# Optimization experiments

Measured on AMD Instinct MI355X. Metric: run time of the kernel, lower is better.

Reference implementation:

```python
import jax, jax.numpy as jnp
import numpy as np


def setup_inputs() -> dict:
    key = jax.random.key(0)
    X = jax.random.normal(key, (8, 64, 64, 64), dtype=jnp.float32)
    return {"X": X}


def reference(X):
    N, C, h, w = X.shape
    x1 = X.reshape(N, C, h * w)            # [N, C, HW]
    x2 = jnp.transpose(x1, (0, 2, 1))      # [N, HW, C]
    scores = jnp.einsum('bnc,bcm->bnm', x2, x1)  # [N, HW, HW]
    c = jax.nn.softmax(scores, axis=2)
    out = jnp.einsum('bnm,bmc->bnc', c, x2)      # [N, HW, C]
    out = jnp.transpose(out, (0, 2, 1)).reshape(N, C, h, w)
    return out
```

## Files before the change

### kernel.cpp

```cpp
#include <hip/hip_runtime.h>
#include <math.h>


#define SEQ 4096
#define DIM 64
#define LDB 72
#define LDO 68
#define LDO2 133
#define LDS2 68
#define QSCALE 1.2011224087864498f

typedef __attribute__((ext_vector_type(8))) short  short8;
typedef __attribute__((ext_vector_type(4))) float  f32x4;

__device__ __forceinline__ unsigned short f2bf(float f) {
    union { float f; unsigned int u; } x; x.f = f;
    unsigned int u = x.u + 0x7FFFu + ((x.u >> 16) & 1u);
    return (unsigned short)(u >> 16);
}
__device__ __forceinline__ float bf2f(unsigned short h) {
    union { unsigned int u; float f; } x; x.u = ((unsigned int)h) << 16; return x.f;
}
__device__ __forceinline__ float fast_exp2(float x) {
#if __has_builtin(__builtin_amdgcn_exp2f)
    return __builtin_amdgcn_exp2f(x);
#else
    float r;
    asm("v_exp_f32 %0, %1\n\ts_nop 0" : "=v"(r) : "v"(x));
    return r;
#endif
}
__device__ __forceinline__ float fast_rcp(float x) {
#if __has_builtin(__builtin_amdgcn_rcpf)
    return __builtin_amdgcn_rcpf(x);
#else
    return 1.f / x;
#endif
}

__global__ __launch_bounds__(256) void prepass4(const float* __restrict__ X,
                                                unsigned short* __restrict__ Kf,
                                                unsigned short* __restrict__ Vf,
                                                float* __restrict__ Norms,
                                                float* __restrict__ MaxPart) {
    __shared__ __align__(16) unsigned short sT[64 * LDS2];
    __shared__ __align__(16) unsigned short sVu[64 * LDS2];
    __shared__ float sRed[4];
    const int b = blockIdx.y, m0 = blockIdx.x * 64;
    const float* Xb = X + (size_t)b * DIM * SEQ;
    const int t = threadIdx.x, w = t >> 6;
    const int mw = t & 15, cg = t >> 4;

    #pragma unroll
    for (int cr = 0; cr < 4; ++cr) {
        const int c = cg * 4 + cr;
        const f32x4 v = *(const f32x4*)(Xb + (size_t)c * SEQ + m0 + 4 * mw);
        *(ushort4*)(sVu + c * LDS2 + 4 * mw) =
            make_ushort4(f2bf(v.x), f2bf(v.y), f2bf(v.z), f2bf(v.w));
        sT[(4 * mw + 0) * LDS2 + c] = f2bf(v.x * QSCALE);
        sT[(4 * mw + 1) * LDS2 + c] = f2bf(v.y * QSCALE);
        sT[(4 * mw + 2) * LDS2 + c] = f2bf(v.z * QSCALE);
        sT[(4 * mw + 3) * LDS2 + c] = f2bf(v.w * QSCALE);
    }
    __syncthreads();
    const int m = t >> 2, ck = t & 3;

    const short8 a0 = *(const short8*)(sT + m * LDS2 + ck * 16);
    const short8 a1 = *(const short8*)(sT + m * LDS2 + ck * 16 + 8);
    {
        const size_t base = (size_t)b * 262144 + (size_t)(m0 >> 5) * 2048;
        #pragma unroll
        for (int j = 0; j < 2; ++j) {
            const int chunk = 2 * ck + j;
            const int tile = m >> 5, mt = (m >> 4) & 1;
            const int quad = chunk & 3, ks = chunk >> 2;
            const size_t off = base + (size_t)(tile * 4 + mt * 2 + ks) * 512
                                    + (size_t)(quad * 16 + (m & 15)) * 8;
            *(short8*)(Kf + off) = j ? a1 : a0;
        }
    }
    float s = 0.f;
    #pragma unroll
    for (int i = 0; i < 8; ++i) {
        const float f0 = bf2f((unsigned short)a0[i]);
        const float f1 = bf2f((unsigned short)a1[i]);
        s += f0 * f0 + f1 * f1;
    }
    s += __shfl_xor(s, 1);
    s += __shfl_xor(s, 2);
    const float nm = sqrtf(s);
    if (ck == 0) Norms[(size_t)b * SEQ + m0 + m] = nm;

    {
        const int ctv = (t >> 6) & 3, lv = t & 63;
        const int qv = lv >> 4, l15v = lv & 15;
        const int cidx = (16 * ctv + l15v) * LDS2;
        const size_t vbase = (size_t)b * 262144 + (size_t)(m0 >> 5) * 2048
                           + (size_t)ctv * 512 + (size_t)lv * 8;
        #pragma unroll
        for (int tl = 0; tl < 2; ++tl) {
            const ushort4 g0 = *(const ushort4*)(sVu + cidx + tl * 32 + 4 * qv);
            const ushort4 g1 = *(const ushort4*)(sVu + cidx + tl * 32 + 16 + 4 * qv);
            union { ushort4 g[2]; short8 v; } cat;
            cat.g[0] = g0; cat.g[1] = g1;
            *(short8*)(Vf + vbase + (size_t)tl * 2048) = cat.v;
        }
    }

    float mx = nm;
    #pragma unroll
    for (int d = 4; d < 64; d <<= 1) mx = fmaxf(mx, __shfl_xor(mx, d));
    if ((t & 63) == 0) sRed[w] = mx;
    __syncthreads();
    if (t == 0)
        MaxPart[b * 64 + blockIdx.x] =
            fmaxf(fmaxf(sRed[0], sRed[1]), fmaxf(sRed[2], sRed[3]));
}

#if __has_builtin(__builtin_amdgcn_global_load_lds)
#define STAGE(BI, SOFF)                                                            \
    {                                                                              \
        unsigned short* dst_ = ring + (BI) * 4096 + (w ? 2048 : 0);                \
        const unsigned short* src_ = (w ? vgp : kgp) + (SOFF);                     \
        _Pragma("unroll")                                                          \
        for (int j_ = 0; j_ < 4; ++j_)                                             \
            __builtin_amdgcn_global_load_lds(                                      \
                (const __attribute__((address_space(1))) unsigned int*)(const void*)(src_ + j_ * 512), \
                (__attribute__((address_space(3))) unsigned int*)(void*)(dst_ + j_ * 512),             \
                16, 0, 0);                                                         \
    }
#else
#define STAGE(BI, SOFF)                                                            \
    {                                                                              \
        unsigned short* dst_ = ring + (BI) * 4096 + (w ? 2048 : 0) + lane * 8;     \
        const unsigned short* src_ = (w ? vgp : kgp) + (SOFF);                     \
        _Pragma("unroll")                                                          \
        for (int j_ = 0; j_ < 4; ++j_)                                             \
            *(short8*)(dst_ + j_ * 512) = *(const short8*)(src_ + j_ * 512);       \
    }
#endif

#define ATTN_STEP(KF, VF)                                                          \
    {                                                                              \
        f32x4 a_[4][2];                                                            \
        _Pragma("unroll")                                                          \
        for (int qt_ = 0; qt_ < 4; ++qt_) {                                        \
            _Pragma("unroll")                                                      \
            for (int mt_ = 0; mt_ < 2; ++mt_) {                                    \
                f32x4 s_ = cin[qt_];                                               \
                s_ = __builtin_amdgcn_mfma_f32_16x16x32_bf16(KF[mt_][0], qf[qt_][0], s_, 0, 0, 0); \
                s_ = __builtin_amdgcn_mfma_f32_16x16x32_bf16(KF[mt_][1], qf[qt_][1], s_, 0, 0, 0); \
                a_[qt_][mt_] = s_;                                                 \
            }                                                                      \
        }                                                                          \
        short8 pa_[4];                                                             \
        _Pragma("unroll")                                                          \
        for (int qt_ = 0; qt_ < 4; ++qt_) {                                        \
            union { unsigned u[4]; short8 v; } pk_;                                \
            _Pragma("unroll")                                                      \
            for (int mt_ = 0; mt_ < 2; ++mt_) {                                    \
                const float p0_ = fast_exp2(a_[qt_][mt_][0]);                      \
                const float p1_ = fast_exp2(a_[qt_][mt_][1]);                      \
                const float p2_ = fast_exp2(a_[qt_][mt_][2]);                      \
                const float p3_ = fast_exp2(a_[qt_][mt_][3]);                      \
                lp4[qt_] += (f32x4){p0_, p1_, p2_, p3_};                           \
                pk_.u[2 * mt_ + 0] = __builtin_amdgcn_perm(__float_as_uint(p1_), __float_as_uint(p0_), 0x07060302u); \
                pk_.u[2 * mt_ + 1] = __builtin_amdgcn_perm(__float_as_uint(p3_), __float_as_uint(p2_), 0x07060302u); \
            }                                                                      \
            pa_[qt_] = pk_.v;                                                      \
        }                                                                          \
        _Pragma("unroll")                                                          \
        for (int qt_ = 0; qt_ < 4; ++qt_) {                                        \
            _Pragma("unroll")                                                      \
            for (int ct_ = 0; ct_ < 4; ++ct_)                                      \
                acc_o[qt_][ct_] = __builtin_amdgcn_mfma_f32_16x16x32_bf16(pa_[qt_], VF[ct_], acc_o[qt_][ct_], 0, 0, 0); \
        }                                                                          \
    }

template <bool PARTIAL>
__global__ __launch_bounds__(128, 2) void attn_split4(const unsigned short* __restrict__ Kf,
                                                      const unsigned short* __restrict__ Vf,
                                                      const float* __restrict__ Norms,
                                                      const float* __restrict__ MaxPart,
                                                      unsigned short* __restrict__ Obf,
                                                      float* __restrict__ Lbase,
                                                      float* __restrict__ Out,
                                                      int niter) {
    __shared__ __align__(16) unsigned char smem[34048];
    unsigned short* ring = (unsigned short*)smem;
    float*          sO   = (float*)smem;

    const int tid  = threadIdx.x;
    const int lane = tid & 63;
    const int w    = tid >> 6;
    const int l15  = lane & 15;
    const int quad = lane >> 4;

    const int gid  = blockIdx.x + 32 * (blockIdx.y + 8 * blockIdx.z);
    const int b    = gid & 7;
    const int rest = gid >> 3;
    const int s0   = (rest & 31) * 128;
    const int h    = rest >> 5;
    const int kt0  = h * niter;
    const unsigned short* Kfb = Kf + (size_t)b * 262144;
    const unsigned short* Vfb = Vf + (size_t)b * 262144;

    float mxn = MaxPart[b * 64 + lane];
    #pragma unroll
    for (int d = 1; d < 64; d <<= 1) mxn = fmaxf(mxn, __shfl_xor(mxn, d));

    short8 qf[4][2];
    f32x4 cin[4];
    const int qtile = (s0 + 64 * w) >> 5;
    #pragma unroll
    for (int qt = 0; qt < 4; ++qt) {
        #pragma unroll
        for (int ks = 0; ks < 2; ++ks)
            qf[qt][ks] = *(const short8*)(Kfb
                + (size_t)((qtile + (qt >> 1)) * 4 + (qt & 1) * 2 + ks) * 512 + lane * 8);
        const float mrow = Norms[(size_t)b * SEQ + s0 + 64 * w + 16 * qt + l15] * mxn;
        cin[qt] = (f32x4){-mrow, -mrow, -mrow, -mrow};
    }

    f32x4 acc_o[4][4];
    #pragma unroll
    for (int qt = 0; qt < 4; ++qt)
        #pragma unroll
        for (int ct = 0; ct < 4; ++ct) acc_o[qt][ct] = (f32x4){0.f, 0.f, 0.f, 0.f};
    f32x4 lp4[4];
    #pragma unroll
    for (int qt = 0; qt < 4; ++qt) lp4[qt] = (f32x4){0.f, 0.f, 0.f, 0.f};

    const unsigned short* kgp = Kfb + lane * 8;
    const unsigned short* vgp = Vfb + lane * 8;

    STAGE(0, (size_t)kt0 * 2048);
    __syncthreads();

    for (int it = 0; it < niter; ++it) {
        const int cur = it & 1;
        if (it + 1 < niter)
            STAGE(cur ^ 1, (size_t)(kt0 + it + 1) * 2048);

        const unsigned short* Kb = ring + cur * 4096;
        const unsigned short* Vb = Kb + 2048;
        short8 kf[2][2], vf[4];
        #pragma unroll
        for (int mt = 0; mt < 2; ++mt)
            #pragma unroll
            for (int ks = 0; ks < 2; ++ks)
                kf[mt][ks] = *(const short8*)(Kb + (mt * 2 + ks) * 512 + lane * 8);
        #pragma unroll
        for (int ct = 0; ct < 4; ++ct)
            vf[ct] = *(const short8*)(Vb + ct * 512 + lane * 8);

        ATTN_STEP(kf, vf);
        __syncthreads();
    }

    float lp[4];
    #pragma unroll
    for (int qt = 0; qt < 4; ++qt) {
        lp[qt] = (lp4[qt][0] + lp4[qt][1]) + (lp4[qt][2] + lp4[qt][3]);
        lp[qt] += __shfl_xor(lp[qt], 16);
        lp[qt] += __shfl_xor(lp[qt], 32);
    }

    if (PARTIAL) {
        if (quad == 0) {
            #pragma unroll
            for (int qt = 0; qt < 4; ++qt)
                (Lbase + (size_t)h * 8 * SEQ)[(size_t)b * SEQ + s0 + 64 * w + 16 * qt + l15] = lp[qt];
        }
    } else {
        #pragma unroll
        for (int qt = 0; qt < 4; ++qt) {
            float inv[4];
            #pragma unroll
            for (int r = 0; r < 4; ++r) inv[r] = fast_rcp(__shfl(lp[qt], 4 * quad + r));
            #pragma unroll
            for (int ct = 0; ct < 4; ++ct)
                #pragma unroll
                for (int r = 0; r < 4; ++r) acc_o[qt][ct][r] *= inv[r];
        }
    }

    __syncthreads();
    #pragma unroll
    for (int qt = 0; qt < 4; ++qt)
        #pragma unroll
        for (int ct = 0; ct < 4; ++ct) {
            const int c = 16 * ct + l15;
            #pragma unroll
            for (int r = 0; r < 4; ++r)
                sO[c * LDO2 + 64 * w + 16 * qt + 4 * quad + r] = acc_o[qt][ct][r];
        }
    __syncthreads();
    const int mw = tid & 31, cg = tid >> 5;
    if (PARTIAL) {
        unsigned short* Op = Obf + (size_t)h * 8 * DIM * SEQ;
        #pragma unroll
        for (int cc = 0; cc < 16; ++cc) {
            const int c = cg + 4 * cc;
            const f32x4 v = *(const f32x4*)(sO + c * LDO2 + 4 * mw);
            *(ushort4*)(Op + ((size_t)b * DIM + c) * SEQ + s0 + 4 * mw) =
                make_ushort4(f2bf(v.x), f2bf(v.y), f2bf(v.z), f2bf(v.w));
        }
    } else {
        #pragma unroll
        for (int cc = 0; cc < 16; ++cc) {
            const int c = cg + 4 * cc;
            const f32x4 v = *(const f32x4*)(sO + c * LDO2 + 4 * mw);
            *(f32x4*)(Out + ((size_t)b * DIM + c) * SEQ + s0 + 4 * mw) = v;
        }
    }
}

__global__ __launch_bounds__(256) void combine4(const unsigned short* __restrict__ Obf,
                                                const float* __restrict__ Lp,
                                                float* __restrict__ Out) {
    const int gid = blockIdx.x * 256 + threadIdx.x;
    const size_t base = (size_t)gid * 4;
    const int s = (int)(base & 4095);
    const int b = (int)(base >> 18);
    f32x4 os = (f32x4){0.f, 0.f, 0.f, 0.f};
    f32x4 ls = (f32x4){0.f, 0.f, 0.f, 0.f};
    #pragma unroll
    for (int h = 0; h < 4; ++h) {
        const ushort4 o = *(const ushort4*)(Obf + (size_t)h * 2097152 + base);
        os[0] += bf2f(o.x); os[1] += bf2f(o.y); os[2] += bf2f(o.z); os[3] += bf2f(o.w);
        const f32x4 l = *(const f32x4*)(Lp + (size_t)h * 8 * SEQ + b * SEQ + s);
        #pragma unroll
        for (int i = 0; i < 4; ++i) ls[i] += l[i];
    }
    f32x4 o;
    #pragma unroll
    for (int i = 0; i < 4; ++i) o[i] = os[i] / ls[i];
    *(f32x4*)(Out + base) = o;
}

__global__ __launch_bounds__(256, 2) void attn_fallback(const float* __restrict__ X,
                                                        float* __restrict__ Out) {
    __shared__ __align__(16) unsigned char smem[27648];
    unsigned short* sK = (unsigned short*)smem;
    unsigned short* sV = (unsigned short*)(smem + 9216);
    unsigned short* sP = (unsigned short*)(smem + 18432);
    float*          sO = (float*)smem;
    const int tid  = threadIdx.x;
    const int lane = tid & 63;
    const int w    = tid >> 6;
    const int l15  = lane & 15;
    const int quad = lane >> 4;
    const int b  = blockIdx.y;
    const int s0 = blockIdx.x * 64;
    const float* Xb = X + (size_t)b * DIM * SEQ;
    const int mgrp = tid & 15;
    const int c0   = tid >> 4;

    for (int cc = 0; cc < 4; ++cc) {
        int c = c0 + 16 * cc;
        const f32x4 v = *(const f32x4*)(Xb + (size_t)c * SEQ + s0 + 4 * mgrp);
        sK[(4 * mgrp + 0) * LDB + c] = f2bf(v.x);
        sK[(4 * mgrp + 1) * LDB + c] = f2bf(v.y);
        sK[(4 * mgrp + 2) * LDB + c] = f2bf(v.z);
        sK[(4 * mgrp + 3) * LDB + c] = f2bf(v.w);
    }
    __syncthreads();
    short8 qf0, qf1;
    {
        const int row = 16 * w + l15;
        qf0 = *(const short8*)(sK + row * LDB + quad * 8);
        qf1 = *(const short8*)(sK + row * LDB + 32 + quad * 8);
    }
    __syncthreads();
    f32x4 acc_o[4];
    for (int ct = 0; ct < 4; ++ct) acc_o[ct] = (f32x4){0.f, 0.f, 0.f, 0.f};
    float m_i[4] = {-1e30f, -1e30f, -1e30f, -1e30f};
    float l_i[4] = {0.f, 0.f, 0.f, 0.f};
    for (int kt = 0; kt < SEQ / 64; ++kt) {
        const int m0 = kt * 64;
        for (int cc = 0; cc < 4; ++cc) {
            int c = c0 + 16 * cc;
            const f32x4 v = *(const f32x4*)(Xb + (size_t)c * SEQ + m0 + 4 * mgrp);
            unsigned short h0 = f2bf(v.x), h1 = f2bf(v.y), h2 = f2bf(v.z), h3 = f2bf(v.w);
            *(ushort4*)(sV + c * LDB + 4 * mgrp) = make_ushort4(h0, h1, h2, h3);
            sK[(4 * mgrp + 0) * LDB + c] = h0;
            sK[(4 * mgrp + 1) * LDB + c] = h1;
            sK[(4 * mgrp + 2) * LDB + c] = h2;
            sK[(4 * mgrp + 3) * LDB + c] = h3;
        }
        __syncthreads();
        short8 vf[2][4];
        for (int ks = 0; ks < 2; ++ks)
            for (int ct = 0; ct < 4; ++ct)
                vf[ks][ct] = *(const short8*)(sV + (16 * ct + l15) * LDB + ks * 32 + quad * 8);
        f32x4 acc_s[4];
        for (int mt = 0; mt < 4; ++mt) {
            const int row = 16 * mt + l15;
            const short8 kf0 = *(const short8*)(sK + row * LDB + quad * 8);
            const short8 kf1 = *(const short8*)(sK + row * LDB + 32 + quad * 8);
            f32x4 a = (f32x4){0.f, 0.f, 0.f, 0.f};
            a = __builtin_amdgcn_mfma_f32_16x16x32_bf16(qf0, kf0, a, 0, 0, 0);
            a = __builtin_amdgcn_mfma_f32_16x16x32_bf16(qf1, kf1, a, 0, 0, 0);
            acc_s[mt] = a;
        }
        float alpha[4];
        for (int r = 0; r < 4; ++r) {
            float mx = fmaxf(fmaxf(acc_s[0][r], acc_s[1][r]), fmaxf(acc_s[2][r], acc_s[3][r]));
            mx = fmaxf(mx, __shfl_xor(mx, 1));
            mx = fmaxf(mx, __shfl_xor(mx, 2));
            mx = fmaxf(mx, __shfl_xor(mx, 4));
            mx = fmaxf(mx, __shfl_xor(mx, 8));
            const float mnew = fmaxf(m_i[r], mx);
            alpha[r] = __expf(m_i[r] - mnew);
            m_i[r] = mnew;
        }
        float rowsum[4] = {0.f, 0.f, 0.f, 0.f};
        unsigned short pb[4][4];
        for (int mt = 0; mt < 4; ++mt)
            for (int r = 0; r < 4; ++r) {
                const float p = __expf(acc_s[mt][r] - m_i[r]);
                rowsum[r] += p;
                pb[mt][r] = f2bf(p);
            }
        for (int r = 0; r < 4; ++r) {
            float s = rowsum[r];
            s += __shfl_xor(s, 1);
            s += __shfl_xor(s, 2);
            s += __shfl_xor(s, 4);
            s += __shfl_xor(s, 8);
            l_i[r] = alpha[r] * l_i[r] + s;
        }
        for (int ct = 0; ct < 4; ++ct)
            for (int r = 0; r < 4; ++r)
                acc_o[ct][r] *= alpha[r];
        for (int mt = 0; mt < 4; ++mt)
            for (int r = 0; r < 4; ++r)
                sP[(16 * w + quad * 4 + r) * LDB + l15 + 16 * mt] = pb[mt][r];
        __syncthreads();
        const short8 pf0 = *(const short8*)(sP + (16 * w + l15) * LDB + quad * 8);
        const short8 pf1 = *(const short8*)(sP + (16 * w + l15) * LDB + 32 + quad * 8);
        for (int ct = 0; ct < 4; ++ct) {
            acc_o[ct] = __builtin_amdgcn_mfma_f32_16x16x32_bf16(pf0, vf[0][ct], acc_o[ct], 0, 0, 0);
            acc_o[ct] = __builtin_amdgcn_mfma_f32_16x16x32_bf16(pf1, vf[1][ct], acc_o[ct], 0, 0, 0);
        }
    }
    float inv[4];
    for (int r = 0; r < 4; ++r) inv[r] = 1.f / l_i[r];
    for (int ct = 0; ct < 4; ++ct) {
        const int c = 16 * ct + l15;
        for (int r = 0; r < 4; ++r)
            sO[c * LDO + 16 * w + quad * 4 + r] = acc_o[ct][r] * inv[r];
    }
    __syncthreads();
    for (int cc = 0; cc < 4; ++cc) {
        const int c = c0 + 16 * cc;
        const f32x4 v = *(const f32x4*)(sO + c * LDO + 4 * mgrp);
        *(f32x4*)(Out + (size_t)b * DIM * SEQ + (size_t)c * SEQ + s0 + 4 * mgrp) = v;
    }
}

extern "C" void kernel_launch(void* const* d_in, const int* in_sizes, int n_in,
                              void* d_out, int out_size, void* d_ws, size_t ws_size,
                              hipStream_t stream) {
    const float* X = (const float*)d_in[0];
    float* Out = (float*)d_out;
    const size_t elems = (size_t)8 * SEQ * DIM;
    const size_t offVf    = elems * 2;
    const size_t offNorms = offVf + elems * 2;
    const size_t offMaxP  = offNorms + (size_t)8 * SEQ * 4;
    const size_t offObf   = offMaxP + 8 * 64 * 4;
    const size_t offLp    = offObf + 4 * elems * 2;
    const size_t need     = offLp + 4 * (size_t)8 * SEQ * 4;

    if (ws_size >= need) {
        unsigned short* Kf = (unsigned short*)d_ws;
        unsigned short* Vf = (unsigned short*)((char*)d_ws + offVf);
        float* Norms   = (float*)((char*)d_ws + offNorms);
        float* MaxPart = (float*)((char*)d_ws + offMaxP);
        unsigned short* Obf = (unsigned short*)((char*)d_ws + offObf);
        float* Lp = (float*)((char*)d_ws + offLp);
        prepass4<<<dim3(64, 8), 256, 0, stream>>>(X, Kf, Vf, Norms, MaxPart);
        attn_split4<true><<<dim3(32, 8, 4), 128, 0, stream>>>(Kf, Vf, Norms, MaxPart,
                                                              Obf, Lp, nullptr, 32);
        combine4<<<(int)(elems / 1024), 256, 0, stream>>>(Obf, Lp, Out);
    } else {
        attn_fallback<<<dim3(64, 8), 256, 0, stream>>>(X, Out);
    }
}
```

Before: 106.9 us.

## Switch attention MFMA from 16x16x32 to 32x32x16 bf16 tiles

Reworks the attention inner loop to use 32x32x16 bf16 MFMA instructions instead of 16x16x32. The K/V fragment layouts written by the prep kernel, the Q fragments, the softmax packing, the row-sum reductions and the output scatter all change to match the 32x32 accumulator layout. The aim is fewer MFMA issues and fragment loads per tile, plus fewer shuffles in the reduction. The cost is larger 16-wide accumulators that raise register pressure, and a broad layout change that must stay consistent across both kernels.

```diff
diff --git a/kernel.cpp b/kernel.cpp
--- a/kernel.cpp
+++ b/kernel.cpp
@@ -10,8 +10,9 @@
 #define LDS2 68
 #define QSCALE 1.2011224087864498f
 
-typedef __attribute__((ext_vector_type(8))) short  short8;
-typedef __attribute__((ext_vector_type(4))) float  f32x4;
+typedef __attribute__((ext_vector_type(8)))  short short8;
+typedef __attribute__((ext_vector_type(4)))  float f32x4;
+typedef __attribute__((ext_vector_type(16))) float f32x16;
 
 __device__ __forceinline__ unsigned short f2bf(float f) {
     union { float f; unsigned int u; } x; x.f = f;
@@ -63,54 +64,59 @@
         sT[(4 * mw + 3) * LDS2 + c] = f2bf(v.w * QSCALE);
     }
     __syncthreads();
-    const int m = t >> 2, ck = t & 3;
-
-    const short8 a0 = *(const short8*)(sT + m * LDS2 + ck * 16);
-    const short8 a1 = *(const short8*)(sT + m * LDS2 + ck * 16 + 8);
+
     {
-        const size_t base = (size_t)b * 262144 + (size_t)(m0 >> 5) * 2048;
-        #pragma unroll
-        for (int j = 0; j < 2; ++j) {
-            const int chunk = 2 * ck + j;
-            const int tile = m >> 5, mt = (m >> 4) & 1;
-            const int quad = chunk & 3, ks = chunk >> 2;
-            const size_t off = base + (size_t)(tile * 4 + mt * 2 + ks) * 512
-                                    + (size_t)(quad * 16 + (m & 15)) * 8;
-            *(short8*)(Kf + off) = j ? a1 : a0;
-        }
-    }
-    float s = 0.f;
-    #pragma unroll
-    for (int i = 0; i < 8; ++i) {
-        const float f0 = bf2f((unsigned short)a0[i]);
-        const float f1 = bf2f((unsigned short)a1[i]);
-        s += f0 * f0 + f1 * f1;
-    }
-    s += __shfl_xor(s, 1);
-    s += __shfl_xor(s, 2);
-    const float nm = sqrtf(s);
-    if (ck == 0) Norms[(size_t)b * SEQ + m0 + m] = nm;
+        const int l = t & 63, ch = t >> 6;
+        const int l31 = l & 31, hi = l >> 5;
+        #pragma unroll
+        for (int tl = 0; tl < 2; ++tl) {
+            const short8 a = *(const short8*)(sT + (tl * 32 + l31) * LDS2 + ch * 16 + hi * 8);
+            const size_t off = (size_t)b * 262144
+                             + (size_t)(((m0 >> 5) + tl) * 4 + ch) * 512 + (size_t)l * 8;
+            *(short8*)(Kf + off) = a;
+        }
+    }
 
     {
-        const int ctv = (t >> 6) & 3, lv = t & 63;
-        const int qv = lv >> 4, l15v = lv & 15;
-        const int cidx = (16 * ctv + l15v) * LDS2;
-        const size_t vbase = (size_t)b * 262144 + (size_t)(m0 >> 5) * 2048
-                           + (size_t)ctv * 512 + (size_t)lv * 8;
+        const int m = t >> 2, ck = t & 3;
+        const short8 a0 = *(const short8*)(sT + m * LDS2 + ck * 16);
+        const short8 a1 = *(const short8*)(sT + m * LDS2 + ck * 16 + 8);
+        float s = 0.f;
+        #pragma unroll
+        for (int i = 0; i < 8; ++i) {
+            const float f0 = bf2f((unsigned short)a0[i]);
+            const float f1 = bf2f((unsigned short)a1[i]);
+            s += f0 * f0 + f1 * f1;
+        }
+        s += __shfl_xor(s, 1);
+        s += __shfl_xor(s, 2);
+        const float nm = sqrtf(s);
+        if (ck == 0) Norms[(size_t)b * SEQ + m0 + m] = nm;
+
+        float mx = nm;
+        #pragma unroll
+        for (int d = 4; d < 64; d <<= 1) mx = fmaxf(mx, __shfl_xor(mx, d));
+        if ((t & 63) == 0) sRed[w] = mx;
+    }
+
+    {
+        const int l = t & 63, pc = t >> 6;
+        const int p = pc >> 1, ct = pc & 1;
+        const int l31 = l & 31, hi = l >> 5;
+        const int crow = (ct * 32 + l31) * LDS2;
         #pragma unroll
         for (int tl = 0; tl < 2; ++tl) {
-            const ushort4 g0 = *(const ushort4*)(sVu + cidx + tl * 32 + 4 * qv);
-            const ushort4 g1 = *(const ushort4*)(sVu + cidx + tl * 32 + 16 + 4 * qv);
+            const int kbase = tl * 32 + p * 16 + hi * 4;
+            const ushort4 g0 = *(const ushort4*)(sVu + crow + kbase);
+            const ushort4 g1 = *(const ushort4*)(sVu + crow + kbase + 8);
             union { ushort4 g[2]; short8 v; } cat;
             cat.g[0] = g0; cat.g[1] = g1;
-            *(short8*)(Vf + vbase + (size_t)tl * 2048) = cat.v;
-        }
-    }
-
-    float mx = nm;
-    #pragma unroll
-    for (int d = 4; d < 64; d <<= 1) mx = fmaxf(mx, __shfl_xor(mx, d));
-    if ((t & 63) == 0) sRed[w] = mx;
+            const size_t off = (size_t)b * 262144
+                             + (size_t)(((m0 >> 5) + tl) * 4 + p * 2 + ct) * 512 + (size_t)l * 8;
+            *(short8*)(Vf + off) = cat.v;
+        }
+    }
+
     __syncthreads();
     if (t == 0)
         MaxPart[b * 64 + blockIdx.x] =
@@ -140,40 +146,46 @@
     }
 #endif
 
-#define ATTN_STEP(KF, VF)                                                          \
+#define ATTN_STEP32(KF, VF)                                                        \
     {                                                                              \
-        f32x4 a_[4][2];                                                            \
+        f32x16 aq0 = cin16[0], aq1 = cin16[1];                                     \
         _Pragma("unroll")                                                          \
-        for (int qt_ = 0; qt_ < 4; ++qt_) {                                        \
+        for (int ch_ = 0; ch_ < 4; ++ch_)                                          \
+            aq0 = __builtin_amdgcn_mfma_f32_32x32x16_bf16(KF[ch_], qf[0][ch_], aq0, 0, 0, 0); \
+        _Pragma("unroll")                                                          \
+        for (int ch_ = 0; ch_ < 4; ++ch_)                                          \
+            aq1 = __builtin_amdgcn_mfma_f32_32x32x16_bf16(KF[ch_], qf[1][ch_], aq1, 0, 0, 0); \
+        short8 pa_[2][2];                                                          \
+        _Pragma("unroll")                                                          \
+        for (int qt_ = 0; qt_ < 2; ++qt_) {                                        \
+            const f32x16 aa_ = qt_ ? aq1 : aq0;                                    \
+            float p_[16];                                                          \
             _Pragma("unroll")                                                      \
-            for (int mt_ = 0; mt_ < 2; ++mt_) {                                    \
-                f32x4 s_ = cin[qt_];                                               \
-                s_ = __builtin_amdgcn_mfma_f32_16x16x32_bf16(KF[mt_][0], qf[qt_][0], s_, 0, 0, 0); \
-                s_ = __builtin_amdgcn_mfma_f32_16x16x32_bf16(KF[mt_][1], qf[qt_][1], s_, 0, 0, 0); \
-                a_[qt_][mt_] = s_;                                                 \
+            for (int r_ = 0; r_ < 16; ++r_) p_[r_] = fast_exp2(aa_[r_]);           \
+            lp4[qt_] += (f32x4){p_[0], p_[1], p_[2], p_[3]};                       \
+            lp4[qt_] += (f32x4){p_[4], p_[5], p_[6], p_[7]};                       \
+            lp4[qt_] += (f32x4){p_[8], p_[9], p_[10], p_[11]};                     \
+            lp4[qt_] += (f32x4){p_[12], p_[13], p_[14], p_[15]};                   \
+            _Pragma("unroll")                                                      \
+            for (int ph_ = 0; ph_ < 2; ++ph_) {                                    \
+                union { unsigned u[4]; short8 v; } pk_;                            \
+                _Pragma("unroll")                                                  \
+                for (int k_ = 0; k_ < 4; ++k_)                                     \
+                    pk_.u[k_] = __builtin_amdgcn_perm(                             \
+                        __float_as_uint(p_[8 * ph_ + 2 * k_ + 1]),                 \
+                        __float_as_uint(p_[8 * ph_ + 2 * k_]), 0x07060302u);       \
+                pa_[qt_][ph_] = pk_.v;                                             \
             }                                                                      \
         }                                                                          \
-        short8 pa_[4];                                                             \
         _Pragma("unroll")                                                          \
-        for (int qt_ = 0; qt_ < 4; ++qt_) {                                        \
-            union { unsigned u[4]; short8 v; } pk_;                                \
+        for (int qt_ = 0; qt_ < 2; ++qt_) {                                        \
             _Pragma("unroll")                                                      \
-            for (int mt_ = 0; mt_ < 2; ++mt_) {                                    \
-                const float p0_ = fast_exp2(a_[qt_][mt_][0]);                      \
-                const float p1_ = fast_exp2(a_[qt_][mt_][1]);                      \
-                const float p2_ = fast_exp2(a_[qt_][mt_][2]);                      \
-                const float p3_ = fast_exp2(a_[qt_][mt_][3]);                      \
-                lp4[qt_] += (f32x4){p0_, p1_, p2_, p3_};                           \
-                pk_.u[2 * mt_ + 0] = __builtin_amdgcn_perm(__float_as_uint(p1_), __float_as_uint(p0_), 0x07060302u); \
-                pk_.u[2 * mt_ + 1] = __builtin_amdgcn_perm(__float_as_uint(p3_), __float_as_uint(p2_), 0x07060302u); \
+            for (int ct_ = 0; ct_ < 2; ++ct_) {                                    \
+                acc_o[qt_][ct_] = __builtin_amdgcn_mfma_f32_32x32x16_bf16(         \
+                    pa_[qt_][0], VF[0][ct_], acc_o[qt_][ct_], 0, 0, 0);            \
+                acc_o[qt_][ct_] = __builtin_amdgcn_mfma_f32_32x32x16_bf16(         \
+                    pa_[qt_][1], VF[1][ct_], acc_o[qt_][ct_], 0, 0, 0);            \
             }                                                                      \
-            pa_[qt_] = pk_.v;                                                      \
-        }                                                                          \
-        _Pragma("unroll")                                                          \
-        for (int qt_ = 0; qt_ < 4; ++qt_) {                                        \
-            _Pragma("unroll")                                                      \
-            for (int ct_ = 0; ct_ < 4; ++ct_)                                      \
-                acc_o[qt_][ct_] = __builtin_amdgcn_mfma_f32_16x16x32_bf16(pa_[qt_], VF[ct_], acc_o[qt_][ct_], 0, 0, 0); \
         }                                                                          \
     }
 
@@ -193,8 +205,8 @@
     const int tid  = threadIdx.x;
     const int lane = tid & 63;
     const int w    = tid >> 6;
-    const int l15  = lane & 15;
-    const int quad = lane >> 4;
+    const int l31  = lane & 31;
+    const int hi   = lane >> 5;
 
     const int gid  = blockIdx.x + 32 * (blockIdx.y + 8 * blockIdx.z);
     const int b    = gid & 7;
@@ -209,27 +221,30 @@
     #pragma unroll
     for (int d = 1; d < 64; d <<= 1) mxn = fmaxf(mxn, __shfl_xor(mxn, d));
 
-    short8 qf[4][2];
-    f32x4 cin[4];
+    short8 qf[2][4];
+    f32x16 cin16[2];
     const int qtile = (s0 + 64 * w) >> 5;
     #pragma unroll
-    for (int qt = 0; qt < 4; ++qt) {
-        #pragma unroll
-        for (int ks = 0; ks < 2; ++ks)
-            qf[qt][ks] = *(const short8*)(Kfb
-                + (size_t)((qtile + (qt >> 1)) * 4 + (qt & 1) * 2 + ks) * 512 + lane * 8);
-        const float mrow = Norms[(size_t)b * SEQ + s0 + 64 * w + 16 * qt + l15] * mxn;
-        cin[qt] = (f32x4){-mrow, -mrow, -mrow, -mrow};
-    }
-
-    f32x4 acc_o[4][4];
-    #pragma unroll
-    for (int qt = 0; qt < 4; ++qt)
-        #pragma unroll
-        for (int ct = 0; ct < 4; ++ct) acc_o[qt][ct] = (f32x4){0.f, 0.f, 0.f, 0.f};
-    f32x4 lp4[4];
-    #pragma unroll
-    for (int qt = 0; qt < 4; ++qt) lp4[qt] = (f32x4){0.f, 0.f, 0.f, 0.f};
+    for (int qt = 0; qt < 2; ++qt) {
+        #pragma unroll
+        for (int ch = 0; ch < 4; ++ch)
+            qf[qt][ch] = *(const short8*)(Kfb
+                + (size_t)((qtile + qt) * 4 + ch) * 512 + lane * 8);
+        const float mrow = Norms[(size_t)b * SEQ + s0 + 64 * w + 32 * qt + l31] * mxn;
+        #pragma unroll
+        for (int r = 0; r < 16; ++r) cin16[qt][r] = -mrow;
+    }
+
+    f32x16 acc_o[2][2];
+    #pragma unroll
+    for (int qt = 0; qt < 2; ++qt)
+        #pragma unroll
+        for (int ct = 0; ct < 2; ++ct)
+            #pragma unroll
+            for (int r = 0; r < 16; ++r) acc_o[qt][ct][r] = 0.f;
+    f32x4 lp4[2];
+    lp4[0] = (f32x4){0.f, 0.f, 0.f, 0.f};
+    lp4[1] = (f32x4){0.f, 0.f, 0.f, 0.f};
 
     const unsigned short* kgp = Kfb + lane * 8;
     const unsigned short* vgp = Vfb + lane * 8;
@@ -244,56 +259,54 @@
 
         const unsigned short* Kb = ring + cur * 4096;
         const unsigned short* Vb = Kb + 2048;
-        short8 kf[2][2], vf[4];
-        #pragma unroll
-        for (int mt = 0; mt < 2; ++mt)
+        short8 kf[4], vf[2][2];
+        #pragma unroll
+        for (int ch = 0; ch < 4; ++ch)
+            kf[ch] = *(const short8*)(Kb + ch * 512 + lane * 8);
+        #pragma unroll
+        for (int p = 0; p < 2; ++p)
             #pragma unroll
-            for (int ks = 0; ks < 2; ++ks)
-                kf[mt][ks] = *(const short8*)(Kb + (mt * 2 + ks) * 512 + lane * 8);
-        #pragma unroll
-        for (int ct = 0; ct < 4; ++ct)
-            vf[ct] = *(const short8*)(Vb + ct * 512 + lane * 8);
-
-        ATTN_STEP(kf, vf);
+            for (int ct = 0; ct < 2; ++ct)
+                vf[p][ct] = *(const short8*)(Vb + (p * 2 + ct) * 512 + lane * 8);
+
+        ATTN_STEP32(kf, vf);
         __syncthreads();
     }
 
-    float lp[4];
-    #pragma unroll
-    for (int qt = 0; qt < 4; ++qt) {
+    float lp[2];
+    #pragma unroll
+    for (int qt = 0; qt < 2; ++qt) {
         lp[qt] = (lp4[qt][0] + lp4[qt][1]) + (lp4[qt][2] + lp4[qt][3]);
-        lp[qt] += __shfl_xor(lp[qt], 16);
         lp[qt] += __shfl_xor(lp[qt], 32);
     }
 
     if (PARTIAL) {
-        if (quad == 0) {
+        if (hi == 0) {
             #pragma unroll
-            for (int qt = 0; qt < 4; ++qt)
-                (Lbase + (size_t)h * 8 * SEQ)[(size_t)b * SEQ + s0 + 64 * w + 16 * qt + l15] = lp[qt];
+            for (int qt = 0; qt < 2; ++qt)
+                (Lbase + (size_t)h * 8 * SEQ)[(size_t)b * SEQ + s0 + 64 * w + 32 * qt + l31] = lp[qt];
         }
     } else {
         #pragma unroll
-        for (int qt = 0; qt < 4; ++qt) {
-            float inv[4];
+        for (int qt = 0; qt < 2; ++qt) {
             #pragma unroll
-            for (int r = 0; r < 4; ++r) inv[r] = fast_rcp(__shfl(lp[qt], 4 * quad + r));
+            for (int r = 0; r < 16; ++r) {
+                const float inv = fast_rcp(__shfl(lp[qt], (r & 3) + 8 * (r >> 2) + 4 * hi));
+                #pragma unroll
+                for (int ct = 0; ct < 2; ++ct) acc_o[qt][ct][r] *= inv;
+            }
+        }
+    }
+
+    __syncthreads();
+    #pragma unroll
+    for (int qt = 0; qt < 2; ++qt)
+        #pragma unroll
+        for (int ct = 0; ct < 2; ++ct) {
+            const int c = ct * 32 + l31;
             #pragma unroll
-            for (int ct = 0; ct < 4; ++ct)
-                #pragma unroll
-                for (int r = 0; r < 4; ++r) acc_o[qt][ct][r] *= inv[r];
-        }
-    }
-
-    __syncthreads();
-    #pragma unroll
-    for (int qt = 0; qt < 4; ++qt)
-        #pragma unroll
-        for (int ct = 0; ct < 4; ++ct) {
-            const int c = 16 * ct + l15;
-            #pragma unroll
-            for (int r = 0; r < 4; ++r)
-                sO[c * LDO2 + 64 * w + 16 * qt + 4 * quad + r] = acc_o[qt][ct][r];
+            for (int r = 0; r < 16; ++r)
+                sO[c * LDO2 + 64 * w + 32 * qt + (r & 3) + 8 * (r >> 2) + 4 * hi] = acc_o[qt][ct][r];
         }
     __syncthreads();
     const int mw = tid & 31, cg = tid >> 5;
```

Result: slower. 109.0 us (+2.0%).
